# Optimization experiments

Measured on AMD Instinct MI355X. Metric: run time of the kernel, lower is better.

## Reference

```python
import jax, jax.numpy as jnp
import numpy as np

IN, OUT, RANK = 512, 1024, 8
STEPS = 8  # fixed-step RK4 integration of the geodesic ODE over t in [0, 1]


def setup_inputs() -> dict:
    key = jax.random.key(0)
    ks = jax.random.split(key, 8)
    scale = 0.05
    x = jax.random.normal(ks[0], (8, 4096, IN), jnp.float32)
    # orthogonal init of U_0 [OUT, IN] (orthonormal columns, tall matrix)
    U0 = jnp.linalg.qr(jax.random.normal(ks[1], (OUT, IN), jnp.float32))[0]
    Wa = scale * jax.random.normal(ks[2], (IN, RANK), jnp.float32)
    La = scale * jax.random.normal(ks[3], (IN, RANK), jnp.float32)
    Ra = scale * jax.random.normal(ks[4], (IN, RANK), jnp.float32)
    Wb = scale * jax.random.normal(ks[5], (IN, RANK), jnp.float32)
    Lb = scale * jax.random.normal(ks[6], (OUT - IN, RANK), jnp.float32)
    Rb = scale * jax.random.normal(ks[7], (IN, RANK), jnp.float32)
    return {"x": x, "U0": U0, "Wa": Wa, "La": La, "Ra": Ra,
            "Wb": Wb, "Lb": Lb, "Rb": Rb}


def _geodesic_solve(U0, A, G):
    # Integrate dU/dt = U @ A + G, U(0) = U0, with RK4 over unit time.
    dt = 1.0 / STEPS
    f = lambda U: U @ A + G
    def step(U, _):
        k1 = f(U)
        k2 = f(U + 0.5 * dt * k1)
        k3 = f(U + 0.5 * dt * k2)
        k4 = f(U + dt * k3)
        return U + (dt / 6.0) * (k1 + 2.0 * k2 + 2.0 * k3 + k4), None
    U, _ = jax.lax.scan(step, U0, None, length=STEPS)
    return U


def reference(x, U0, Wa, La, Ra, Wb, Lb, Rb):
    # z: pooled context [B, IN]
    z = x.mean(axis=1)
    # low-rank controller -> skew-symmetric Lie-algebra drift A [IN, IN]
    a = z @ Wa                                      # [B, R]
    A = jnp.einsum('br,ir,jr->bij', a, La, Ra)      # [B, IN, IN]
    A_avg = (A - jnp.swapaxes(A, 1, 2)).mean(axis=0)  # skew, batch-averaged
    # low-rank forcing B [B, OUT-IN, IN], batch-averaged
    b = z @ Wb                                      # [B, R]
    B_avg = jnp.einsum('br,or,jr->boj', b, Lb, Rb).mean(axis=0)
    # pad top with zeros -> G [OUT, IN]
    G = jnp.concatenate([jnp.zeros((IN, IN), x.dtype), B_avg], axis=0)
    # geodesic/Lie ODE solve for the dynamic weight W [OUT, IN]
    W = _geodesic_solve(U0, A_avg, G)
    # final dense projection
    return x @ W.T
```

## Files before the change

kernel.cpp:

```cpp
#include <hip/hip_runtime.h>
#include <hip/hip_bf16.h>
#include <type_traits>
#include <cstdint>

#define IN_DIM   512
#define OUT_DIM  1024
#define MROWS    32768

typedef float f32x4 __attribute__((ext_vector_type(4)));
typedef short s8vec __attribute__((ext_vector_type(8)));
typedef __bf16 b8vec __attribute__((ext_vector_type(8)));

template <typename V, typename = void>
struct mfma_ok : std::false_type {};
template <typename V>
struct mfma_ok<V, std::void_t<decltype(__builtin_amdgcn_mfma_f32_16x16x32_bf16(
    std::declval<V>(), std::declval<V>(), std::declval<f32x4>(), 0, 0, 0))>>
    : std::true_type {};
using frag_t = std::conditional_t<mfma_ok<s8vec>::value, s8vec, b8vec>;

__device__ __forceinline__ void async_copy16(void* lds, const void* g) {
    __builtin_amdgcn_global_load_lds(
        (const __attribute__((address_space(1))) void*)(uintptr_t)g,
        (__attribute__((address_space(3))) void*)(uint32_t)(uintptr_t)lds,
        16, 0, 0);
}

__device__ __forceinline__ unsigned short f2bf(float f) {
    unsigned int u = __float_as_uint(f);
    unsigned int r = (u + 0x7fffu + ((u >> 16) & 1u)) >> 16;
    return (unsigned short)r;
}

__global__ void __launch_bounds__(256) geo_k1(const float* __restrict__ x,
                                              unsigned short* __restrict__ xh,
                                              const float* __restrict__ Wa,
                                              const float* __restrict__ Wb,
                                              float* __restrict__ part) {
    const int tid  = threadIdx.x;
    const int c4   = (tid & 127) * 4;
    const int half = tid >> 7;
    const int r0   = blockIdx.x * 32 + half * 16;
    float4 s = {0.f, 0.f, 0.f, 0.f};
    for (int i = 0; i < 16; ++i) {
        const size_t base = (size_t)(r0 + i) * IN_DIM + c4;
        float4 v = *(const float4*)(x + base);
        s.x += v.x; s.y += v.y; s.z += v.z; s.w += v.w;
        ushort4 h;
        h.x = f2bf(v.x); h.y = f2bf(v.y); h.z = f2bf(v.z); h.w = f2bf(v.w);
        *(ushort4*)(xh + base) = h;
    }
    const float* wa = Wa + (size_t)c4 * 8;
    const float* wb = Wb + (size_t)c4 * 8;
    float av[8], bv[8];
#pragma unroll
    for (int r = 0; r < 8; ++r) {
        av[r] = s.x * wa[r] + s.y * wa[8 + r] + s.z * wa[16 + r] + s.w * wa[24 + r];
        bv[r] = s.x * wb[r] + s.y * wb[8 + r] + s.z * wb[16 + r] + s.w * wb[24 + r];
    }
#pragma unroll
    for (int off = 32; off; off >>= 1) {
#pragma unroll
        for (int r = 0; r < 8; ++r) {
            av[r] += __shfl_xor(av[r], off, 64);
            bv[r] += __shfl_xor(bv[r], off, 64);
        }
    }
    __shared__ float wred[4][16];
    const int lane = tid & 63, wave = tid >> 6;
    if (lane == 0) {
#pragma unroll
        for (int r = 0; r < 8; ++r) { wred[wave][r] = av[r]; wred[wave][8 + r] = bv[r]; }
    }
    __syncthreads();
    if (tid < 16)
        part[(size_t)blockIdx.x * 16 + tid] =
            wred[0][tid] + wred[1][tid] + wred[2][tid] + wred[3][tid];
}

__device__ __forceinline__ void mm16(float (*D)[16], float (*A)[16], float (*B)[16]) {
    const int tid = threadIdx.x;
    const int i = tid >> 4, j = tid & 15;
    float s = 0.f;
#pragma unroll
    for (int k = 0; k < 16; ++k) s += A[i][k] * B[k][j];
    __syncthreads();
    D[i][j] = s;
    __syncthreads();
}

__global__ void __launch_bounds__(256) geo_k2(const float* __restrict__ part,
                                              const float* __restrict__ La,
                                              const float* __restrict__ Ra,
                                              const float* __restrict__ Lb,
                                              const float* __restrict__ Rb,
                                              float* __restrict__ Vws,
                                              float* __restrict__ Lbp,
                                              float* __restrict__ VPws,
                                              float* __restrict__ RRws) {
    __shared__ float sV[IN_DIM][16];
    __shared__ float sRb[IN_DIM][8];
    __shared__ float red2[16][16];
    __shared__ float gs[16];
    __shared__ float G16[16][16], Jm[16][16];
    __shared__ float C2m[16][16], C3m[16][16], C4m[16][16];
    __shared__ float Cp[16][16], Cq[16][16];
    __shared__ float Pi[16][16], Xi[16][16], T1[16][16], T2[16][16], Ct[16][16];
    __shared__ float Zm[8][16], Em[8][16];
    const int tid = threadIdx.x;
    const int i = tid >> 4, j = tid & 15;

    {
        const int u = tid & 15, c = tid >> 4;
        float s = 0.f;
        for (int q = 0; q < 64; ++q) s += part[(size_t)(c * 64 + q) * 16 + u];
        red2[c][u] = s;
    }
    __syncthreads();
    if (tid < 16) {
        float s = 0.f;
#pragma unroll
        for (int c = 0; c < 16; ++c) s += red2[c][tid];
        gs[tid] = s * (1.0f / 32768.0f);
    }
    __syncthreads();

    for (int rr = 0; rr < 2; ++rr) {
        const int row = tid * 2 + rr;
#pragma unroll
        for (int r = 0; r < 8; ++r) {
            const float vl = gs[r] * La[row * 8 + r];
            const float vr = Ra[row * 8 + r];
            sV[row][r]     = vl;
            sV[row][8 + r] = vr;
            Vws[row * 16 + r]     = vl;
            Vws[row * 16 + 8 + r] = vr;
            sRb[row][r] = Rb[row * 8 + r];
            Lbp[row * 8 + r] = gs[8 + r] * Lb[row * 8 + r];
        }
    }
    __syncthreads();

    {
        float s = 0.f;
        for (int k = 0; k < IN_DIM; ++k) s += sV[k][i] * sV[k][j];
        G16[i][j] = s;
        float jm = 0.f;
        if (i < 8 && j == i + 8) jm = 1.f;
        if (i >= 8 && j == i - 8) jm = -1.f;
        Jm[i][j] = jm;
    }
    if (tid < 128) {
        const int r = tid >> 4, u = tid & 15;
        float s = 0.f;
        for (int k = 0; k < IN_DIM; ++k) s += sRb[k][r] * sV[k][u];
        Zm[r][u] = s;
    }
    __syncthreads();

    mm16(T1, Jm, G16);  mm16(C2m, T1, Jm);
    mm16(T1, C2m, G16); mm16(C3m, T1, Jm);
    mm16(T1, C3m, G16); mm16(C4m, T1, Jm);

    const float h  = 0.125f;
    const float c1 = h, c2 = h * h * 0.5f, c3 = h * h * h * (1.f / 6.f),
                c4 = h * h * h * h * (1.f / 24.f);
    Cp[i][j] = c1 * Jm[i][j] + c2 * C2m[i][j] + c3 * C3m[i][j] + c4 * C4m[i][j];
    Cq[i][j] = c2 * Jm[i][j] + c3 * C2m[i][j] + c4 * C3m[i][j];
    Xi[i][j] = 0.f;
    __syncthreads();
    Pi[i][j] = Cp[i][j];
    __syncthreads();

    for (int it = 0; it < 7; ++it) {
        mm16(T1, Pi, G16);
        mm16(T2, T1, Cp);
        const float pij = Pi[i][j];
        Xi[i][j] += pij;
        Pi[i][j] = pij + Cp[i][j] + T2[i][j];
        __syncthreads();
    }

    mm16(T1, Cq, G16);
    mm16(T2, T1, Xi);
    Ct[i][j] = 8.f * Cq[i][j] + h * Xi[i][j] + T2[i][j];
    __syncthreads();

    if (tid < 128) {
        const int r = tid >> 4, u = tid & 15;
        float s = 0.f;
#pragma unroll
        for (int t = 0; t < 16; ++t) s += Zm[r][t] * Ct[t][u];
        Em[r][u] = s;
    }
    __syncthreads();

#pragma unroll
    for (int rr = 0; rr < 2; ++rr) {
        const int row = tid * 2 + rr;
        float v[16];
#pragma unroll
        for (int k = 0; k < 16; ++k) v[k] = sV[row][k];
#pragma unroll
        for (int u = 0; u < 16; ++u) {
            float s = 0.f;
#pragma unroll
            for (int k = 0; k < 16; ++k) s += v[k] * Pi[k][u];
            VPws[row * 16 + u] = s;
        }
#pragma unroll
        for (int r = 0; r < 8; ++r) {
            float s = sRb[row][r];
#pragma unroll
            for (int u = 0; u < 16; ++u) s += Em[r][u] * v[u];
            RRws[r * IN_DIM + row] = s;
        }
    }
}

__global__ void __launch_bounds__(256) geo_k34(const float* __restrict__ U0,
                                               const float* __restrict__ Vws,
                                               const float* __restrict__ VPws,
                                               const float* __restrict__ Lbp,
                                               const float* __restrict__ RRws,
                                               unsigned short* __restrict__ wh) {
    const int o   = blockIdx.x;
    const int tid = threadIdx.x;
    const int j0  = tid * 2;
    const float2 u0 = *(const float2*)(U0 + (size_t)o * IN_DIM + j0);

    const float* vpa = VPws + j0 * 16;
    const float* vpb = vpa + 16;
    float p[16];
#pragma unroll
    for (int u = 0; u < 16; ++u) p[u] = u0.x * vpa[u] + u0.y * vpb[u];
#pragma unroll
    for (int off = 32; off; off >>= 1) {
#pragma unroll
        for (int u = 0; u < 16; ++u) p[u] += __shfl_xor(p[u], off, 64);
    }
    __shared__ float wred[4][16];
    __shared__ float sY[16];
    const int lane = tid & 63, wave = tid >> 6;
    if (lane == 0) {
#pragma unroll
        for (int u = 0; u < 16; ++u) wred[wave][u] = p[u];
    }
    __syncthreads();
    if (tid < 16) sY[tid] = wred[0][tid] + wred[1][tid] + wred[2][tid] + wred[3][tid];
    __syncthreads();

    const float* va = Vws + j0 * 16;
    const float* vb = va + 16;
    float w0 = u0.x, w1 = u0.y;
#pragma unroll
    for (int u = 0; u < 16; ++u) {
        const float s = sY[u];
        w0 += s * va[u];
        w1 += s * vb[u];
    }
    if (o >= IN_DIM) {
        const int op = o - IN_DIM;
#pragma unroll
        for (int r = 0; r < 8; ++r) {
            const float lb = Lbp[op * 8 + r];
            w0 += lb * RRws[r * IN_DIM + j0];
            w1 += lb * RRws[r * IN_DIM + j0 + 1];
        }
    }
    ushort2 hv;
    hv.x = f2bf(w0); hv.y = f2bf(w1);
    *(ushort2*)(wh + (size_t)o * IN_DIM + j0) = hv;
}

__device__ __forceinline__ void k5_frag_loads(const char* lds, int sb, int aoff, int boff,
                                              frag_t (&a)[8], frag_t (&b)[4]) {
#pragma unroll
    for (int u = 0; u < 8; ++u)
        a[u] = *(const frag_t*)(lds + sb + aoff + u * 1024);
#pragma unroll
    for (int s = 0; s < 4; ++s)
        b[s] = *(const frag_t*)(lds + sb + boff + s * 1024);
}

template <int VM, bool DO_STAGE>
__device__ __forceinline__ void k5_step(char* lds, int t,
                                        const __hip_bfloat16* gA0, const __hip_bfloat16* gA1,
                                        const __hip_bfloat16* gB0, const __hip_bfloat16* gB1,
                                        int ldsA0, int ldsA1, int aoff, int boff,
                                        f32x4 (&acc)[8][4]) {
    if constexpr (VM == 12)     asm volatile("s_waitcnt vmcnt(12)" ::: "memory");
    else if constexpr (VM == 8) asm volatile("s_waitcnt vmcnt(8)"  ::: "memory");
    else if constexpr (VM == 4) asm volatile("s_waitcnt vmcnt(4)"  ::: "memory");
    else                        asm volatile("s_waitcnt vmcnt(0)"  ::: "memory");
    __builtin_amdgcn_s_barrier();
    __builtin_amdgcn_sched_barrier(0);

    const int sb = (t & 3) * 32768;
    frag_t a[8], b[4];
    k5_frag_loads(lds, sb, aoff, boff, a, b);

    __builtin_amdgcn_s_setprio(1);
#pragma unroll
    for (int u = 0; u < 8; ++u)
#pragma unroll
        for (int s = 0; s < 4; ++s)
            acc[u][s] = __builtin_amdgcn_mfma_f32_16x16x32_bf16(a[u], b[s], acc[u][s], 0, 0, 0);
    __builtin_amdgcn_s_setprio(0);

    asm volatile("s_waitcnt lgkmcnt(0)" ::: "memory");
    __builtin_amdgcn_sched_barrier(0);
    __builtin_amdgcn_s_barrier();

    if constexpr (DO_STAGE) {
        const int ko = (t + 4) * 32;
        async_copy16(lds + sb + ldsA0,         gA0 + ko);
        async_copy16(lds + sb + ldsA1,         gA1 + ko);
        async_copy16(lds + sb + 16384 + ldsA0, gB0 + ko);
        async_copy16(lds + sb + 16384 + ldsA1, gB1 + ko);
    }
}

__global__ void __launch_bounds__(512, 2) geo_k5_gemm(const __hip_bfloat16* __restrict__ A,
                                                      const __hip_bfloat16* __restrict__ B,
                                                      float* __restrict__ C) {
    __shared__ alignas(16) char lds[131072];
    const int tid = threadIdx.x;
    const int l = tid & 63, w = tid >> 6;

    const int bid = blockIdx.x;
    const int xcd = bid & 7;
    const int loc = bid >> 3;
    const int m0  = (xcd * 16 + (loc >> 2)) * 256;
    const int n0  = (loc & 3) * 256;

    const int swz   = (((l & 3) ^ ((l >> 3) & 3)) * 8);
    const int rloc0 = w * 32 + (l >> 2);
    const int rloc1 = rloc0 + 16;
    const __hip_bfloat16* gA0 = A + (size_t)(m0 + rloc0) * IN_DIM + swz;
    const __hip_bfloat16* gA1 = A + (size_t)(m0 + rloc1) * IN_DIM + swz;
    const __hip_bfloat16* gB0 = B + (size_t)(n0 + rloc0) * IN_DIM + swz;
    const __hip_bfloat16* gB1 = B + (size_t)(n0 + rloc1) * IN_DIM + swz;
    const int ldsA0 = w * 2048 + l * 16;
    const int ldsA1 = ldsA0 + 1024;

    const int lane15 = l & 15;
    const int s_r    = (lane15 >> 1) & 3;
    const int rdch   = ((l >> 4) ^ s_r) * 16;
    const int wmoff  = (w >> 2) * 128;
    const int wnoff  = (w & 3) * 64;
    const int aoff   = (wmoff + lane15) * 64 + rdch;
    const int boff   = 16384 + (wnoff + lane15) * 64 + rdch;

    f32x4 acc[8][4];
#pragma unroll
    for (int u = 0; u < 8; ++u)
#pragma unroll
        for (int s = 0; s < 4; ++s) acc[u][s] = (f32x4){0.f, 0.f, 0.f, 0.f};

#pragma unroll
    for (int p = 0; p < 4; ++p) {
        const int sb = p * 32768;
        const int ko = p * 32;
        async_copy16(lds + sb + ldsA0,         gA0 + ko);
        async_copy16(lds + sb + ldsA1,         gA1 + ko);
        async_copy16(lds + sb + 16384 + ldsA0, gB0 + ko);
        async_copy16(lds + sb + 16384 + ldsA1, gB1 + ko);
    }

    for (int t = 0; t < 12; ++t)
        k5_step<12, true>(lds, t, gA0, gA1, gB0, gB1, ldsA0, ldsA1, aoff, boff, acc);
    k5_step<12, false>(lds, 12, gA0, gA1, gB0, gB1, ldsA0, ldsA1, aoff, boff, acc);
    k5_step<8,  false>(lds, 13, gA0, gA1, gB0, gB1, ldsA0, ldsA1, aoff, boff, acc);
    k5_step<4,  false>(lds, 14, gA0, gA1, gB0, gB1, ldsA0, ldsA1, aoff, boff, acc);
    k5_step<0,  false>(lds, 15, gA0, gA1, gB0, gB1, ldsA0, ldsA1, aoff, boff, acc);

    const int cm = m0 + wmoff + (l >> 4) * 4;
    const int cn = n0 + wnoff + lane15;
#pragma unroll
    for (int u = 0; u < 8; ++u)
#pragma unroll
        for (int s = 0; s < 4; ++s)
#pragma unroll
            for (int v = 0; v < 4; ++v)
                C[(size_t)(cm + u * 16 + v) * OUT_DIM + cn + s * 16] = acc[u][s][v];
}

extern "C" void kernel_launch(void* const* d_in, const int* in_sizes, int n_in,
                              void* d_out, int out_size, void* d_ws, size_t ws_size,
                              hipStream_t stream) {
    const float* x  = (const float*)d_in[0];
    const float* U0 = (const float*)d_in[1];
    const float* Wa = (const float*)d_in[2];
    const float* La = (const float*)d_in[3];
    const float* Ra = (const float*)d_in[4];
    const float* Wb = (const float*)d_in[5];
    const float* Lb = (const float*)d_in[6];
    const float* Rb = (const float*)d_in[7];
    float* out = (float*)d_out;

    char* ws = (char*)d_ws;
    unsigned short* xh  = (unsigned short*)(ws);
    unsigned short* wh  = (unsigned short*)(ws + 33554432);
    float* part = (float*)(ws + 34603008);
    float* Vws  = (float*)(ws + 34668544);
    float* Lbp  = (float*)(ws + 34701312);
    float* RRws = (float*)(ws + 34717696);
    float* VPws = (float*)(ws + 34734080);

    geo_k1<<<1024, 256, 0, stream>>>(x, xh, Wa, Wb, part);
    geo_k2<<<1, 256, 0, stream>>>(part, La, Ra, Lb, Rb, Vws, Lbp, VPws, RRws);
    geo_k34<<<1024, 256, 0, stream>>>(U0, Vws, VPws, Lbp, RRws, wh);
    geo_k5_gemm<<<512, 512, 0, stream>>>((const __hip_bfloat16*)xh,
                                         (const __hip_bfloat16*)wh, out);
}
```

Baseline: 272.7 us.

## Restructure geo_k2 small-matrix math with split-K Gram, vectorized LDS, fewer barriers

Rewrites the single-block geo_k2 setup kernel. The partial-sum reduction and the Gram matrices G16 and Zm now use split-K over all 256 threads, with float4 LDS reads and 4x4 register tiles, replacing the serial 512-long dot products. Multiplications by the J permutation matrix become index swaps and sign flips. The 16x16 products use padded, transposed row-dot layouts so fewer __syncthreads are needed. The intent is to shorten this serial, latency-bound kernel that runs ahead of the main GEMM, at the cost of extra LDS scratch and more complex indexing.

New measurement: 263.3 us (median of 2 runs). 1.04x faster.

```diff
diff --git a/kernel.cpp b/kernel.cpp
--- a/kernel.cpp
+++ b/kernel.cpp
@@ -78,15 +78,15 @@
             wred[0][tid] + wred[1][tid] + wred[2][tid] + wred[3][tid];
 }
 
-__device__ __forceinline__ void mm16(float (*D)[16], float (*A)[16], float (*B)[16]) {
-    const int tid = threadIdx.x;
-    const int i = tid >> 4, j = tid & 15;
+__device__ __forceinline__ float rowdot16(const float* a, const float* b) {
     float s = 0.f;
 #pragma unroll
-    for (int k = 0; k < 16; ++k) s += A[i][k] * B[k][j];
-    __syncthreads();
-    D[i][j] = s;
-    __syncthreads();
+    for (int c = 0; c < 4; ++c) {
+        f32x4 av = *(const f32x4*)(a + 4 * c);
+        f32x4 bv = *(const f32x4*)(b + 4 * c);
+        s += av[0] * bv[0] + av[1] * bv[1] + av[2] * bv[2] + av[3] * bv[3];
+    }
+    return s;
 }
 
 __global__ void __launch_bounds__(256) geo_k2(const float* __restrict__ part,
@@ -98,22 +98,36 @@
                                               float* __restrict__ Lbp,
                                               float* __restrict__ VPws,
                                               float* __restrict__ RRws) {
-    __shared__ float sV[IN_DIM][16];
-    __shared__ float sRb[IN_DIM][8];
-    __shared__ float red2[16][16];
+    __shared__ __align__(16) float sV[IN_DIM][16];
+    __shared__ __align__(16) float sRb[IN_DIM][8];
+    __shared__ __align__(16) float scratch[8192];
+    __shared__ __align__(16) float red2[16][16];
     __shared__ float gs[16];
-    __shared__ float G16[16][16], Jm[16][16];
-    __shared__ float C2m[16][16], C3m[16][16], C4m[16][16];
-    __shared__ float Cp[16][16], Cq[16][16];
-    __shared__ float Pi[16][16], Xi[16][16], T1[16][16], T2[16][16], Ct[16][16];
-    __shared__ float Zm[8][16], Em[8][16];
+    __shared__ __align__(16) float G16[16][20], C2m[16][20], C3m[16][20], C4m[16][20];
+    __shared__ __align__(16) float Cp[16][20], CpT[16][20], Cq[16][20];
+    __shared__ __align__(16) float Pi[16][20], Xi[16][20], XiT[16][20];
+    __shared__ __align__(16) float T1m[16][20], CtT[16][20];
+    __shared__ __align__(16) float Zm[8][16];
+    __shared__ __align__(16) float EmT[16][8];
     const int tid = threadIdx.x;
     const int i = tid >> 4, j = tid & 15;
 
     {
-        const int u = tid & 15, c = tid >> 4;
+        const float4* p4 = (const float4*)part;
+        float4 a = {0.f, 0.f, 0.f, 0.f};
+#pragma unroll
+        for (int q = 0; q < 16; ++q) {
+            float4 v = p4[tid + 256 * q];
+            a.x += v.x; a.y += v.y; a.z += v.z; a.w += v.w;
+        }
+        *(float4*)&scratch[(tid >> 2) * 16 + (tid & 3) * 4] = a;
+    }
+    __syncthreads();
+    {
+        const int c = tid >> 4, u = tid & 15;
         float s = 0.f;
-        for (int q = 0; q < 64; ++q) s += part[(size_t)(c * 64 + q) * 16 + u];
+#pragma unroll
+        for (int q = 0; q < 4; ++q) s += scratch[(c * 4 + q) * 16 + u];
         red2[c][u] = s;
     }
     __syncthreads();
@@ -125,95 +139,193 @@
     }
     __syncthreads();
 
+#pragma unroll
     for (int rr = 0; rr < 2; ++rr) {
         const int row = tid * 2 + rr;
-#pragma unroll
-        for (int r = 0; r < 8; ++r) {
-            const float vl = gs[r] * La[row * 8 + r];
-            const float vr = Ra[row * 8 + r];
-            sV[row][r]     = vl;
-            sV[row][8 + r] = vr;
-            Vws[row * 16 + r]     = vl;
-            Vws[row * 16 + 8 + r] = vr;
-            sRb[row][r] = Rb[row * 8 + r];
-            Lbp[row * 8 + r] = gs[8 + r] * Lb[row * 8 + r];
-        }
-    }
-    __syncthreads();
-
+        float4 la0 = *(const float4*)(La + row * 8);
+        float4 la1 = *(const float4*)(La + row * 8 + 4);
+        float4 ra0 = *(const float4*)(Ra + row * 8);
+        float4 ra1 = *(const float4*)(Ra + row * 8 + 4);
+        float4 rb0 = *(const float4*)(Rb + row * 8);
+        float4 rb1 = *(const float4*)(Rb + row * 8 + 4);
+        float4 lb0 = *(const float4*)(Lb + row * 8);
+        float4 lb1 = *(const float4*)(Lb + row * 8 + 4);
+        float4 v0 = {gs[0] * la0.x, gs[1] * la0.y, gs[2] * la0.z, gs[3] * la0.w};
+        float4 v1 = {gs[4] * la1.x, gs[5] * la1.y, gs[6] * la1.z, gs[7] * la1.w};
+        *(float4*)&sV[row][0]  = v0;
+        *(float4*)&sV[row][4]  = v1;
+        *(float4*)&sV[row][8]  = ra0;
+        *(float4*)&sV[row][12] = ra1;
+        *(float4*)(Vws + row * 16)      = v0;
+        *(float4*)(Vws + row * 16 + 4)  = v1;
+        *(float4*)(Vws + row * 16 + 8)  = ra0;
+        *(float4*)(Vws + row * 16 + 12) = ra1;
+        *(float4*)&sRb[row][0] = rb0;
+        *(float4*)&sRb[row][4] = rb1;
+        float4 l0 = {gs[8] * lb0.x,  gs[9] * lb0.y,  gs[10] * lb0.z, gs[11] * lb0.w};
+        float4 l1 = {gs[12] * lb1.x, gs[13] * lb1.y, gs[14] * lb1.z, gs[15] * lb1.w};
+        *(float4*)(Lbp + row * 8)     = l0;
+        *(float4*)(Lbp + row * 8 + 4) = l1;
+    }
+    __syncthreads();
+
+    {
+        const int ks = tid >> 4, blk = tid & 15, bi = blk >> 2, bj = blk & 3;
+        float acc[4][4] = {};
+        for (int q = 0; q < 32; ++q) {
+            const int k = ks * 32 + ((q + ks) & 31);
+            f32x4 a = *(const f32x4*)&sV[k][bi * 4];
+            f32x4 b = *(const f32x4*)&sV[k][bj * 4];
+#pragma unroll
+            for (int r = 0; r < 4; ++r)
+#pragma unroll
+                for (int c = 0; c < 4; ++c) acc[r][c] += a[r] * b[c];
+        }
+#pragma unroll
+        for (int r = 0; r < 4; ++r) {
+            f32x4 t = {acc[r][0], acc[r][1], acc[r][2], acc[r][3]};
+            *(f32x4*)&scratch[ks * 256 + (bi * 4 + r) * 16 + bj * 4] = t;
+        }
+        const int zks = tid >> 3, zblk = tid & 7, zbi = zblk >> 2, zbj = zblk & 3;
+        float zacc[4][4] = {};
+        for (int q = 0; q < 16; ++q) {
+            const int k = zks * 16 + ((q + zks) & 15);
+            f32x4 a = *(const f32x4*)&sRb[k][zbi * 4];
+            f32x4 b = *(const f32x4*)&sV[k][zbj * 4];
+#pragma unroll
+            for (int r = 0; r < 4; ++r)
+#pragma unroll
+                for (int c = 0; c < 4; ++c) zacc[r][c] += a[r] * b[c];
+        }
+#pragma unroll
+        for (int r = 0; r < 4; ++r) {
+            f32x4 t = {zacc[r][0], zacc[r][1], zacc[r][2], zacc[r][3]};
+            *(f32x4*)&scratch[4096 + zks * 128 + (zbi * 4 + r) * 16 + zbj * 4] = t;
+        }
+    }
+    __syncthreads();
     {
         float s = 0.f;
-        for (int k = 0; k < IN_DIM; ++k) s += sV[k][i] * sV[k][j];
+#pragma unroll
+        for (int ks = 0; ks < 16; ++ks) s += scratch[ks * 256 + i * 16 + j];
         G16[i][j] = s;
-        float jm = 0.f;
-        if (i < 8 && j == i + 8) jm = 1.f;
-        if (i >= 8 && j == i - 8) jm = -1.f;
-        Jm[i][j] = jm;
     }
     if (tid < 128) {
         const int r = tid >> 4, u = tid & 15;
         float s = 0.f;
-        for (int k = 0; k < IN_DIM; ++k) s += sRb[k][r] * sV[k][u];
+#pragma unroll
+        for (int ks = 0; ks < 32; ++ks) s += scratch[4096 + ks * 128 + r * 16 + u];
         Zm[r][u] = s;
     }
     __syncthreads();
 
-    mm16(T1, Jm, G16);  mm16(C2m, T1, Jm);
-    mm16(T1, C2m, G16); mm16(C3m, T1, Jm);
-    mm16(T1, C3m, G16); mm16(C4m, T1, Jm);
+    C2m[i][j] = (((i ^ j) & 8) ? 1.f : -1.f) * G16[i ^ 8][j ^ 8];
+    __syncthreads();
+    {
+        float s = rowdot16(&C2m[i][0], &G16[j][0]);
+        C3m[i][j ^ 8] = (j < 8) ? s : -s;
+    }
+    __syncthreads();
+    {
+        float s = rowdot16(&C3m[i][0], &G16[j][0]);
+        C4m[i][j ^ 8] = (j < 8) ? s : -s;
+    }
+    __syncthreads();
 
     const float h  = 0.125f;
     const float c1 = h, c2 = h * h * 0.5f, c3 = h * h * h * (1.f / 6.f),
                 c4 = h * h * h * h * (1.f / 24.f);
-    Cp[i][j] = c1 * Jm[i][j] + c2 * C2m[i][j] + c3 * C3m[i][j] + c4 * C4m[i][j];
-    Cq[i][j] = c2 * Jm[i][j] + c3 * C2m[i][j] + c4 * C3m[i][j];
-    Xi[i][j] = 0.f;
-    __syncthreads();
-    Pi[i][j] = Cp[i][j];
+    {
+        const float jm = (j == (i ^ 8)) ? ((i < 8) ? 1.f : -1.f) : 0.f;
+        const float cp = c1 * jm + c2 * C2m[i][j] + c3 * C3m[i][j] + c4 * C4m[i][j];
+        const float cq = c2 * jm + c3 * C2m[i][j] + c4 * C3m[i][j];
+        Cp[i][j] = cp; CpT[j][i] = cp; Cq[i][j] = cq;
+        Xi[i][j] = 0.f; XiT[i][j] = 0.f;
+        Pi[i][j] = cp;
+    }
     __syncthreads();
 
     for (int it = 0; it < 7; ++it) {
-        mm16(T1, Pi, G16);
-        mm16(T2, T1, Cp);
+        T1m[i][j] = rowdot16(&Pi[i][0], &G16[j][0]);
+        __syncthreads();
+        const float t2  = rowdot16(&T1m[i][0], &CpT[j][0]);
         const float pij = Pi[i][j];
-        Xi[i][j] += pij;
-        Pi[i][j] = pij + Cp[i][j] + T2[i][j];
+        Xi[i][j] += pij; XiT[j][i] += pij;
+        Pi[i][j] = pij + Cp[i][j] + t2;
         __syncthreads();
     }
 
-    mm16(T1, Cq, G16);
-    mm16(T2, T1, Xi);
-    Ct[i][j] = 8.f * Cq[i][j] + h * Xi[i][j] + T2[i][j];
+    T1m[i][j] = rowdot16(&Cq[i][0], &G16[j][0]);
+    __syncthreads();
+    {
+        const float t2 = rowdot16(&T1m[i][0], &XiT[j][0]);
+        const float ct = 8.f * Cq[i][j] + h * Xi[i][j] + t2;
+        CtT[j][i] = ct;
+    }
     __syncthreads();
 
     if (tid < 128) {
         const int r = tid >> 4, u = tid & 15;
-        float s = 0.f;
-#pragma unroll
-        for (int t = 0; t < 16; ++t) s += Zm[r][t] * Ct[t][u];
-        Em[r][u] = s;
-    }
-    __syncthreads();
-
-#pragma unroll
-    for (int rr = 0; rr < 2; ++rr) {
-        const int row = tid * 2 + rr;
-        float v[16];
-#pragma unroll
-        for (int k = 0; k < 16; ++k) v[k] = sV[row][k];
+        EmT[u][r] = rowdot16(&Zm[r][0], &CtT[u][0]);
+    }
+    __syncthreads();
+
+    {
+        const int row0 = tid * 2, row1 = row0 + 1;
+        float v0a[16], v1a[16];
+#pragma unroll
+        for (int c = 0; c < 4; ++c) {
+            f32x4 t0 = *(const f32x4*)&sV[row0][c * 4];
+            f32x4 t1 = *(const f32x4*)&sV[row1][c * 4];
+#pragma unroll
+            for (int q = 0; q < 4; ++q) { v0a[c * 4 + q] = t0[q]; v1a[c * 4 + q] = t1[q]; }
+        }
+        float o0[16] = {}, o1[16] = {};
+#pragma unroll
+        for (int k = 0; k < 16; ++k) {
+            f32x4 p0 = *(const f32x4*)&Pi[k][0];
+            f32x4 p1 = *(const f32x4*)&Pi[k][4];
+            f32x4 p2 = *(const f32x4*)&Pi[k][8];
+            f32x4 p3 = *(const f32x4*)&Pi[k][12];
+            const float a = v0a[k], b = v1a[k];
+#pragma unroll
+            for (int q = 0; q < 4; ++q) {
+                o0[q]      += a * p0[q];  o1[q]      += b * p0[q];
+                o0[4 + q]  += a * p1[q];  o1[4 + q]  += b * p1[q];
+                o0[8 + q]  += a * p2[q];  o1[8 + q]  += b * p2[q];
+                o0[12 + q] += a * p3[q];  o1[12 + q] += b * p3[q];
+            }
+        }
+#pragma unroll
+        for (int c = 0; c < 4; ++c) {
+            f32x4 w0 = {o0[c * 4], o0[c * 4 + 1], o0[c * 4 + 2], o0[c * 4 + 3]};
+            f32x4 w1 = {o1[c * 4], o1[c * 4 + 1], o1[c * 4 + 2], o1[c * 4 + 3]};
+            *(f32x4*)(VPws + row0 * 16 + c * 4) = w0;
+            *(f32x4*)(VPws + row1 * 16 + c * 4) = w1;
+        }
+        float s0[8], s1[8];
+#pragma unroll
+        for (int c = 0; c < 2; ++c) {
+            f32x4 t0 = *(const f32x4*)&sRb[row0][c * 4];
+            f32x4 t1 = *(const f32x4*)&sRb[row1][c * 4];
+#pragma unroll
+            for (int q = 0; q < 4; ++q) { s0[c * 4 + q] = t0[q]; s1[c * 4 + q] = t1[q]; }
+        }
 #pragma unroll
         for (int u = 0; u < 16; ++u) {
-            float s = 0.f;
-#pragma unroll
-            for (int k = 0; k < 16; ++k) s += v[k] * Pi[k][u];
-            VPws[row * 16 + u] = s;
+            f32x4 e0 = *(const f32x4*)&EmT[u][0];
+            f32x4 e1 = *(const f32x4*)&EmT[u][4];
+            const float a = v0a[u], b = v1a[u];
+#pragma unroll
+            for (int r = 0; r < 4; ++r) {
+                s0[r]     += a * e0[r];  s1[r]     += b * e0[r];
+                s0[4 + r] += a * e1[r];  s1[4 + r] += b * e1[r];
+            }
         }
 #pragma unroll
         for (int r = 0; r < 8; ++r) {
-            float s = sRb[row][r];
-#pragma unroll
-            for (int u = 0; u < 16; ++u) s += Em[r][u] * v[u];
-            RRws[r * IN_DIM + row] = s;
+            RRws[r * IN_DIM + row0] = s0[r];
+            RRws[r * IN_DIM + row1] = s1[r];
         }
     }
 }
```
